# Kernel optimization log

Hardware: AMD Instinct MI355X
Metric: run time of the kernel (lower is better)

The kernel has to match this reference:

```python
import jax, jax.numpy as jnp
import numpy as np

# dims
B, A, CIN, CC = 512, 256, 7, 16          # batch, num_actions, input channels, conv channels
D, H, DH, E = 48, 8, 6, 512              # token_dimension, heads, head_dim, num_embeddings
S, T = 32, 32                            # num_input_tokens, num_output_tokens
AH = H * DH                              # 48
NL = 4                                   # attention layers
CONV_IN = A * CC                         # 4096
ENC = S * D                              # 1536
DEC_OUT = A * CIN                        # 1792
SCALE = float(np.sqrt(D))                # module uses sqrt(input_embedding_dim)
EPS = 1e-5


def _ln(x, g, b):
    m = jnp.mean(x, axis=-1, keepdims=True)
    v = jnp.var(x, axis=-1, keepdims=True)
    return (x - m) * jax.lax.rsqrt(v + EPS) * g + b


def setup_inputs() -> dict:
    key = jax.random.key(0)
    ks = iter(jax.random.split(key, 64))
    def rn(shape, s=0.05):
        return jax.random.normal(next(ks), shape, dtype=jnp.float32) * s
    inp = {}
    inp['x'] = jax.random.normal(next(ks), (B, A, CIN), dtype=jnp.float32)
    inp['u'] = jax.random.uniform(next(ks), (T, B), dtype=jnp.float32)
    inp['bn_g'] = jnp.ones((CIN,), jnp.float32); inp['bn_b'] = jnp.zeros((CIN,), jnp.float32)
    inp['conv_w'] = rn((CC, CIN, 5)); inp['conv_b'] = jnp.zeros((CC,), jnp.float32)
    inp['tk_W1'] = rn((CONV_IN, 2 * CONV_IN)); inp['tk_b1'] = jnp.zeros((2 * CONV_IN,), jnp.float32)
    inp['tk_W2'] = rn((2 * CONV_IN, ENC)); inp['tk_b2'] = jnp.zeros((ENC,), jnp.float32)
    for nm in ('q', 'k', 'v'):
        inp['ln%s_g' % nm] = jnp.ones((NL, D), jnp.float32)
        inp['ln%s_b' % nm] = jnp.zeros((NL, D), jnp.float32)
        inp['W%s' % nm] = rn((NL, D, AH))
        inp['b%s' % nm] = jnp.zeros((NL, AH), jnp.float32)
    inp['Wo'] = rn((NL, AH, D)); inp['bo'] = jnp.zeros((NL, D), jnp.float32)
    inp['mln_g'] = jnp.ones((NL, D), jnp.float32); inp['mln_b'] = jnp.zeros((NL, D), jnp.float32)
    inp['W1'] = rn((NL, D, 2 * D)); inp['b1'] = jnp.zeros((NL, 2 * D), jnp.float32)
    inp['W2'] = rn((NL, 2 * D, D)); inp['b2'] = jnp.zeros((NL, D), jnp.float32)
    inp['emb'] = rn((D, E), 1.0)          # nn.Parameter(torch.randn(D, E))
    inp['pos_enc'] = rn((T, D), 1.0)      # nn.Parameter(torch.randn(T, D))
    inp['dec_W1'] = rn((ENC, 2 * ENC)); inp['dec_b1'] = jnp.zeros((2 * ENC,), jnp.float32)
    inp['dec_W2'] = rn((2 * ENC, DEC_OUT)); inp['dec_b2'] = jnp.zeros((DEC_OUT,), jnp.float32)
    return inp


def _fwd(x, u, bn_g, bn_b, conv_w, conv_b, tk_W1, tk_b1, tk_W2, tk_b2,
         lnq_g, lnq_b, Wq, bq, lnk_g, lnk_b, Wk, bk, lnv_g, lnv_b, Wv, bv, Wo, bo,
         mln_g, mln_b, W1, b1, W2, b2, emb, pos_enc, dec_W1, dec_b1, dec_W2, dec_b2):
    # --- conv stem (BatchNorm1d in training mode: batch statistics) ---
    xt = x.transpose(0, 2, 1)                              # [B, 7, A]
    mu = jnp.mean(xt, axis=(0, 2), keepdims=True)
    var = jnp.var(xt, axis=(0, 2), keepdims=True)
    xn = (xt - mu) * jax.lax.rsqrt(var + EPS) * bn_g[None, :, None] + bn_b[None, :, None]
    xc = jax.lax.conv_general_dilated(xn, conv_w, (1,), ((2, 2),),
                                      dimension_numbers=('NCH', 'OIH', 'NCH')) + conv_b[None, :, None]
    xf = xc.reshape(B, -1)                                 # [B, 16*A]
    h = jax.nn.relu(xf @ tk_W1 + tk_b1)
    toks = (h @ tk_W2 + tk_b2).reshape(B, S, D)            # [B, S, D]

    STOT = S + T
    kc = jnp.zeros((NL, B, H, STOT, DH), jnp.float32)
    vc = jnp.zeros_like(kc)

    # --- prefill pass (output discarded; fills KV caches) ---
    ii = jnp.arange(S)[:, None]; jj = jnp.arange(S)[None, :]
    pre_mask = jnp.where(jj - ii >= S - 1, -999.0, 0.0)    # triu(-999, diagonal=S-1), as in source
    xcur = toks
    for l in range(NL):
        q = (_ln(xcur, lnq_g[l], lnq_b[l]) @ Wq[l] + bq[l]).reshape(B, S, H, DH).transpose(0, 2, 1, 3)
        k = (_ln(xcur, lnk_g[l], lnk_b[l]) @ Wk[l] + bk[l]).reshape(B, S, H, DH).transpose(0, 2, 1, 3)
        v = (_ln(xcur, lnv_g[l], lnv_b[l]) @ Wv[l] + bv[l]).reshape(B, S, H, DH).transpose(0, 2, 1, 3)
        kc = kc.at[l, :, :, :S].set(k)
        vc = vc.at[l, :, :, :S].set(v)
        attn = jax.nn.softmax(jnp.einsum('bhqd,bhkd->bhqk', q, k) / SCALE + pre_mask, axis=-1)
        o = jnp.einsum('bhqk,bhkd->bhqd', attn, v).transpose(0, 2, 1, 3).reshape(B, S, AH)
        xcur = o @ Wo[l] + bo[l] + xcur
        hh = jax.nn.relu(_ln(xcur, mln_g[l], mln_b[l]) @ W1[l] + b1[l])
        xcur = hh @ W2[l] + b2[l]

    jidx = jnp.arange(STOT)

    def step(carry, xs):
        kc, vc = carry
        i, pe, uu = xs
        p = S + i                                          # cache length before this step
        xtk = jnp.broadcast_to(pe, (B, 1, D))
        newk, newv = [], []
        for l in range(NL):
            q = (_ln(xtk, lnq_g[l], lnq_b[l]) @ Wq[l] + bq[l]).reshape(B, 1, H, DH).transpose(0, 2, 1, 3)
            k = (_ln(xtk, lnk_g[l], lnk_b[l]) @ Wk[l] + bk[l]).reshape(B, 1, H, DH).transpose(0, 2, 1, 3)
            v = (_ln(xtk, lnv_g[l], lnv_b[l]) @ Wv[l] + bv[l]).reshape(B, 1, H, DH).transpose(0, 2, 1, 3)
            kcl = jax.lax.dynamic_update_slice(kc[l], k, (0, 0, p, 0))
            vcl = jax.lax.dynamic_update_slice(vc[l], v, (0, 0, p, 0))
            scores = jnp.einsum('bhqd,bhkd->bhqk', q, kcl) / SCALE
            # source mask: -999 added for positions >= mask_offset (includes the new token itself)
            scores = scores + jnp.where(jidx >= p, -999.0, 0.0)
            attn = jax.nn.softmax(scores, axis=-1)
            o = jnp.einsum('bhqk,bhkd->bhqd', attn, vcl).transpose(0, 2, 1, 3).reshape(B, 1, AH)
            xtk = o @ Wo[l] + bo[l] + xtk
            hh = jax.nn.relu(_ln(xtk, mln_g[l], mln_b[l]) @ W1[l] + b1[l])
            xtk = hh @ W2[l] + b2[l]
            newk.append(kcl); newv.append(vcl)
        attended = xtk                                     # [B, 1, D]
        probs = jax.nn.softmax((attended @ emb).reshape(B, E), axis=1)
        cdf = jnp.cumsum(probs, axis=1)
        idx = jnp.clip(jnp.sum((cdf < uu[:, None]).astype(jnp.int32), axis=1), 0, E - 1)
        sel = emb.T[idx].reshape(B, 1, D)
        st = sel + attended - jax.lax.stop_gradient(attended)  # straight-through
        return (jnp.stack(newk), jnp.stack(newv)), st

    (_, _), outs = jax.lax.scan(step, (kc, vc), (jnp.arange(T), pos_enc, u))
    out_tokens = outs.transpose(1, 0, 2, 3).reshape(B, T * D)
    dh_ = jax.nn.relu(out_tokens @ dec_W1 + dec_b1)
    traj = (dh_ @ dec_W2 + dec_b2).reshape(B, A, CIN)
    return traj


def reference(x, u, bn_g, bn_b, conv_w, conv_b, tk_W1, tk_b1, tk_W2, tk_b2,
              lnq_g, lnq_b, Wq, bq, lnk_g, lnk_b, Wk, bk, lnv_g, lnv_b, Wv, bv, Wo, bo,
              mln_g, mln_b, W1, b1, W2, b2, emb, pos_enc, dec_W1, dec_b1, dec_W2, dec_b2):
    return _fwd(x, u, bn_g, bn_b, conv_w, conv_b, tk_W1, tk_b1, tk_W2, tk_b2,
                lnq_g, lnq_b, Wq, bq, lnk_g, lnk_b, Wk, bk, lnv_g, lnv_b, Wv, bv, Wo, bo,
                mln_g, mln_b, W1, b1, W2, b2, emb, pos_enc, dec_W1, dec_b1, dec_W2, dec_b2)
```

## Files before the change

kernel.cpp:

```cpp
#include <hip/hip_runtime.h>

static const double SCALE_ = 6.928203230275509;

__device__ inline float  fma_t(float a, float b, float c)  { return fmaf(a, b, c); }
__device__ inline double fma_t(double a, double b, double c){ return fma(a, b, c); }

__device__ __attribute__((noinline)) double dotW(const double* a,
                                                 const float* W, int n, int ldw,
                                                 double init) {
  double a0 = init, a1 = 0.0;
#pragma unroll 2
  for (int i = 0; i < n; i += 2) {
    a0 = fma(a[i],     (double)W[i * ldw],       a0);
    a1 = fma(a[i + 1], (double)W[(i + 1) * ldw], a1);
  }
  return a0 + a1;
}

template <int N, typename WP>
__device__ __forceinline__ double dotN(const double* a, WP W, int ldw, double init) {
  double c0 = init, c1 = 0.0, c2 = 0.0, c3 = 0.0;
#pragma unroll
  for (int i = 0; i < N; i += 4) {
    c0 = fma(a[i],     (double)W[i * ldw],       c0);
    c1 = fma(a[i + 1], (double)W[(i + 1) * ldw], c1);
    c2 = fma(a[i + 2], (double)W[(i + 2) * ldw], c2);
    c3 = fma(a[i + 3], (double)W[(i + 3) * ldw], c3);
  }
  return (c0 + c1) + (c2 + c3);
}

__device__ __attribute__((noinline)) double2 ln_stats48(const double* x) {
  double s0 = 0, s1 = 0, q0 = 0, q1 = 0;
#pragma unroll 2
  for (int i = 0; i < 48; i += 2) {
    const double va = x[i], vb = x[i + 1];
    s0 += va; q0 = fma(va, va, q0);
    s1 += vb; q1 = fma(vb, vb, q1);
  }
  const double m = (s0 + s1) / 48.0;
  const double rs = 1.0 / sqrt((q0 + q1) / 48.0 - m * m + 1e-5);
  return make_double2(m, rs);
}

__device__ __attribute__((noinline)) double exp_ni(double x) { return exp(x); }

__global__ __launch_bounds__(256) void bn_partial_kernel(const float* __restrict__ x,
                                                         double* __restrict__ part) {
  __shared__ double sh[256 * 14];
  const int tid = threadIdx.x;
  const int idx = blockIdx.x * 256 + tid;
  const float* p = x + (size_t)idx * 7;
  for (int c = 0; c < 7; ++c) {
    double v = (double)p[c];
    sh[tid * 14 + c] = v;
    sh[tid * 14 + 7 + c] = v * v;
  }
  __syncthreads();
  if (tid < 14) {
    double acc = 0.0;
    for (int t = 0; t < 256; ++t) acc += sh[t * 14 + tid];
    part[blockIdx.x * 14 + tid] = acc;
  }
}

__global__ void bn_final_kernel(const double* __restrict__ part,
                                const float* __restrict__ g, const float* __restrict__ bb,
                                double* __restrict__ stat) {
  const int c = threadIdx.x;
  if (c < 7) {
    double s = 0.0, s2 = 0.0;
    for (int i = 0; i < 512; ++i) { s += part[i * 14 + c]; s2 += part[i * 14 + 7 + c]; }
    const double mean = s / 131072.0;
    const double var = s2 / 131072.0 - mean * mean;
    const double rstd = 1.0 / sqrt(var + 1e-5);
    const double scale = rstd * (double)g[c];
    stat[c] = scale;
    stat[7 + c] = (double)bb[c] - mean * scale;
  }
}

__global__ __launch_bounds__(256) void conv_kernel(const float* __restrict__ x,
                                                   const float* __restrict__ wconv,
                                                   const float* __restrict__ cb,
                                                   const double* __restrict__ stat,
                                                   double* __restrict__ xf) {
  __shared__ double wsh[560 + 14];
  const int tid = threadIdx.x;
  for (int i = tid; i < 560; i += 256) wsh[i] = (double)wconv[i];
  for (int i = tid; i < 14; i += 256) wsh[560 + i] = stat[i];
  __syncthreads();
  const int idx = blockIdx.x * 256 + tid;
  const int a = idx & 255;
  const int o = (idx >> 8) & 15;
  const int b = idx >> 12;
  double acc = (double)cb[o];
  const float* xb = x + (size_t)b * (256 * 7);
  for (int k = 0; k < 5; ++k) {
    const int pos = a + k - 2;
    if (pos < 0 || pos >= 256) continue;
    const float* xp = xb + pos * 7;
    for (int ci = 0; ci < 7; ++ci) {
      const double xn = (double)xp[ci] * wsh[560 + ci] + wsh[567 + ci];
      acc = fma(xn, wsh[(o * 7 + ci) * 5 + k], acc);
    }
  }
  xf[idx] = acc;
}

template <typename T, bool BIAS, bool RELU>
__global__ __launch_bounds__(256) void gemm128_kernel(const T* __restrict__ A,
                                                      const float* __restrict__ Bm,
                                                      const float* __restrict__ bias,
                                                      T* __restrict__ C,
                                                      const int M, const int N, const int K,
                                                      const int kc) {
  __shared__ T As[16][130];
  __shared__ T Bs[16][66];
  const int tid = threadIdx.x;
  const int tx = tid & 15, ty = tid >> 4;
  const int n0 = blockIdx.x * 64, m0 = blockIdx.y * 128;
  const int k0 = blockIdx.z * kc, kend = k0 + kc;
  const int ar = tid >> 1, ac = (tid & 1) * 8;
  const int br = tid >> 4, bc = (tid & 15) * 4;
  const T* Ap = A + (size_t)(m0 + ar) * K;
  const float* Bp = Bm + (size_t)br * N + n0 + bc;
  T acc[8][4] = {};
  for (int k = k0; k < kend; k += 16) {
    T av8[8];
#pragma unroll
    for (int i = 0; i < 8; ++i) av8[i] = Ap[k + ac + i];
    const float4 bw = *(const float4*)(Bp + (size_t)k * N);
#pragma unroll
    for (int i = 0; i < 8; ++i) As[ac + i][ar] = av8[i];
    Bs[br][bc] = (T)bw.x; Bs[br][bc + 1] = (T)bw.y;
    Bs[br][bc + 2] = (T)bw.z; Bs[br][bc + 3] = (T)bw.w;
    __syncthreads();
#pragma unroll
    for (int kk = 0; kk < 16; ++kk) {
      T a[8], b[4];
#pragma unroll
      for (int i = 0; i < 8; ++i) a[i] = As[kk][ty * 8 + i];
#pragma unroll
      for (int j = 0; j < 4; ++j) b[j] = Bs[kk][tx * 4 + j];
#pragma unroll
      for (int i = 0; i < 8; ++i)
#pragma unroll
        for (int j = 0; j < 4; ++j) acc[i][j] = fma_t(a[i], b[j], acc[i][j]);
    }
    __syncthreads();
  }
  T* Cp = C + (size_t)blockIdx.z * M * N;
#pragma unroll
  for (int i = 0; i < 8; ++i) {
    const int row = m0 + ty * 8 + i;
#pragma unroll
    for (int j = 0; j < 4; ++j) {
      const int col = n0 + tx * 4 + j;
      T v = acc[i][j];
      if (BIAS) v += (T)bias[col];
      if (RELU) v = v > (T)0 ? v : (T)0;
      Cp[(size_t)row * N + col] = v;
    }
  }
}

template <typename T, bool BIAS, bool RELU>
__global__ __launch_bounds__(256) void gemm_kernel(const T* __restrict__ A,
                                                   const float* __restrict__ Bm,
                                                   const float* __restrict__ bias,
                                                   T* __restrict__ C,
                                                   const int M, const int N, const int K,
                                                   const int kc) {
  __shared__ T As[16][65];
  __shared__ T Bs[16][65];
  const int tid = threadIdx.x;
  const int tx = tid & 15, ty = tid >> 4;
  const int n0 = blockIdx.x * 64, m0 = blockIdx.y * 64;
  const int k0 = blockIdx.z * kc, kend = k0 + kc;
  const int ar = tid >> 2, ac = (tid & 3) * 4;
  const int br = tid >> 4, bc = (tid & 15) * 4;
  const T* Ap = A + (size_t)(m0 + ar) * K;
  const float* Bp = Bm + (size_t)br * N + n0 + bc;
  T acc[4][4] = {};
  for (int k = k0; k < kend; k += 16) {
    const T a0 = Ap[k + ac], a1 = Ap[k + ac + 1], a2 = Ap[k + ac + 2], a3 = Ap[k + ac + 3];
    const float4 bw = *(const float4*)(Bp + (size_t)k * N);
    As[ac][ar] = a0; As[ac + 1][ar] = a1; As[ac + 2][ar] = a2; As[ac + 3][ar] = a3;
    Bs[br][bc] = (T)bw.x; Bs[br][bc + 1] = (T)bw.y; Bs[br][bc + 2] = (T)bw.z; Bs[br][bc + 3] = (T)bw.w;
    __syncthreads();
#pragma unroll
    for (int kk = 0; kk < 16; ++kk) {
      T av[4], bv2[4];
#pragma unroll
      for (int i = 0; i < 4; ++i) av[i] = As[kk][ty * 4 + i];
#pragma unroll
      for (int j = 0; j < 4; ++j) bv2[j] = Bs[kk][tx * 4 + j];
#pragma unroll
      for (int i = 0; i < 4; ++i)
#pragma unroll
        for (int j = 0; j < 4; ++j) acc[i][j] = fma_t(av[i], bv2[j], acc[i][j]);
    }
    __syncthreads();
  }
  T* Cp = C + (size_t)blockIdx.z * M * N;
#pragma unroll
  for (int i = 0; i < 4; ++i) {
    const int row = m0 + ty * 4 + i;
#pragma unroll
    for (int j = 0; j < 4; ++j) {
      const int col = n0 + tx * 4 + j;
      T v = acc[i][j];
      if (BIAS) v += (T)bias[col];
      if (RELU) v = v > (T)0 ? v : (T)0;
      Cp[(size_t)row * N + col] = v;
    }
  }
}

__global__ __launch_bounds__(256) void reduce2_bias_kernel(const double* __restrict__ part,
                                                           const float* __restrict__ bias,
                                                           double* __restrict__ out,
                                                           const int MN, const int N) {
  const int i = blockIdx.x * 256 + threadIdx.x;
  if (i < MN) out[i] = part[i] + part[MN + i] + (double)bias[i % N];
}

__global__ __launch_bounds__(256) void prefill_kernel(
    const double* __restrict__ toks,
    const float* __restrict__ lnq_g, const float* __restrict__ lnq_b,
    const float* __restrict__ Wq, const float* __restrict__ bq,
    const float* __restrict__ lnk_g, const float* __restrict__ lnk_b,
    const float* __restrict__ Wk, const float* __restrict__ bk,
    const float* __restrict__ lnv_g, const float* __restrict__ lnv_b,
    const float* __restrict__ Wv, const float* __restrict__ bvv,
    const float* __restrict__ Wo, const float* __restrict__ bo,
    const float* __restrict__ mln_g, const float* __restrict__ mln_b,
    const float* __restrict__ W1, const float* __restrict__ b1,
    const float* __restrict__ W2, const float* __restrict__ b2,
    double* __restrict__ kcache, double* __restrict__ vcache) {
  const int b = blockIdx.x, tid = threadIdx.x;
  __shared__ double xcur[1536], abuf[1536], qbuf[1536], kvbuf[3072];
  __shared__ double mean[32], rstd[32];
  double* kb = kvbuf;
  double* vb = kvbuf + 1536;

#pragma unroll 1
  for (int i = tid; i < 1536; i += 256) xcur[i] = toks[(size_t)b * 1536 + i];
  __syncthreads();

#pragma unroll 1
  for (int l = 0; l < 4; ++l) {
    if (tid < 32) {
      double s = 0.0, s2 = 0.0;
#pragma unroll 4
      for (int i = 0; i < 48; ++i) { const double v = xcur[tid * 48 + i]; s += v; s2 += v * v; }
      const double m = s / 48.0;
      mean[tid] = m;
      rstd[tid] = 1.0 / sqrt(s2 / 48.0 - m * m + 1e-5);
    }
    __syncthreads();
    const bool last = (l == 3);

    if (!last) {
#pragma unroll 1
      for (int i = tid; i < 1536; i += 256) {
        const int t = i / 48, d = i % 48;
        abuf[i] = (xcur[i] - mean[t]) * rstd[t] * (double)lnq_g[l * 48 + d] + (double)lnq_b[l * 48 + d];
      }
      __syncthreads();
#pragma unroll 1
      for (int i = tid; i < 1536; i += 256) {
        const int t = i / 48, j = i % 48;
        qbuf[i] = dotW(abuf + t * 48, Wq + l * 2304 + j, 48, 48, (double)bq[l * 48 + j]);
      }
      __syncthreads();
    }
#pragma unroll 1
    for (int i = tid; i < 1536; i += 256) {
      const int t = i / 48, d = i % 48;
      abuf[i] = (xcur[i] - mean[t]) * rstd[t] * (double)lnk_g[l * 48 + d] + (double)lnk_b[l * 48 + d];
    }
    __syncthreads();
#pragma unroll 1
    for (int i = tid; i < 1536; i += 256) {
      const int t = i / 48, j = i % 48;
      kb[i] = dotW(abuf + t * 48, Wk + l * 2304 + j, 48, 48, (double)bk[l * 48 + j]);
    }
    __syncthreads();
#pragma unroll 1
    for (int i = tid; i < 1536; i += 256) {
      const int t = i / 48, d = i % 48;
      abuf[i] = (xcur[i] - mean[t]) * rstd[t] * (double)lnv_g[l * 48 + d] + (double)lnv_b[l * 48 + d];
    }
    __syncthreads();
#pragma unroll 1
    for (int i = tid; i < 1536; i += 256) {
      const int t = i / 48, j = i % 48;
      vb[i] = dotW(abuf + t * 48, Wv + l * 2304 + j, 48, 48, (double)bvv[l * 48 + j]);
    }
    __syncthreads();
#pragma unroll 1
    for (int i = tid; i < 1536; i += 256) {
      const int t = i / 48, j = i % 48;
      const int h = j / 6, d = j % 6;
      const size_t ci = ((((size_t)b * 4 + l) * 8 + h) * 64 + t) * 6 + d;
      kcache[ci] = kb[i];
      vcache[ci] = vb[i];
    }

    if (!last) {
      const int t = tid >> 3, h = tid & 7;
      const double* qp = qbuf + t * 48 + h * 6;
      const double q0 = qp[0], q1 = qp[1], q2 = qp[2], q3 = qp[3], q4 = qp[4], q5 = qp[5];
      double mx = -1e300;
#pragma unroll 4
      for (int j = 0; j < 32; ++j) {
        const double* kp = kb + j * 48 + h * 6;
        double sv = q0 * kp[0];
        sv = fma(q1, kp[1], sv); sv = fma(q2, kp[2], sv); sv = fma(q3, kp[3], sv);
        sv = fma(q4, kp[4], sv); sv = fma(q5, kp[5], sv);
        sv /= SCALE_;
        if (t == 0 && j == 31) sv -= 999.0;
        mx = sv > mx ? sv : mx;
      }
      double den = 0, o0 = 0, o1 = 0, o2 = 0, o3 = 0, o4 = 0, o5 = 0;
#pragma unroll 4
      for (int j = 0; j < 32; ++j) {
        const double* kp = kb + j * 48 + h * 6;
        double sv = q0 * kp[0];
        sv = fma(q1, kp[1], sv); sv = fma(q2, kp[2], sv); sv = fma(q3, kp[3], sv);
        sv = fma(q4, kp[4], sv); sv = fma(q5, kp[5], sv);
        sv /= SCALE_;
        if (t == 0 && j == 31) sv -= 999.0;
        const double e = exp_ni(sv - mx);
        den += e;
        const double* vp = vb + j * 48 + h * 6;
        o0 = fma(e, vp[0], o0); o1 = fma(e, vp[1], o1); o2 = fma(e, vp[2], o2);
        o3 = fma(e, vp[3], o3); o4 = fma(e, vp[4], o4); o5 = fma(e, vp[5], o5);
      }
      abuf[t * 48 + h * 6 + 0] = o0 / den;
      abuf[t * 48 + h * 6 + 1] = o1 / den;
      abuf[t * 48 + h * 6 + 2] = o2 / den;
      abuf[t * 48 + h * 6 + 3] = o3 / den;
      abuf[t * 48 + h * 6 + 4] = o4 / den;
      abuf[t * 48 + h * 6 + 5] = o5 / den;
      __syncthreads();
#pragma unroll 1
      for (int i = tid; i < 1536; i += 256) {
        const int t2 = i / 48, j = i % 48;
        xcur[i] += dotW(abuf + t2 * 48, Wo + l * 2304 + j, 48, 48, (double)bo[l * 48 + j]);
      }
      __syncthreads();
      if (tid < 32) {
        double s = 0.0, s2 = 0.0;
#pragma unroll 4
        for (int i = 0; i < 48; ++i) { const double v = xcur[tid * 48 + i]; s += v; s2 += v * v; }
        const double m = s / 48.0;
        mean[tid] = m;
        rstd[tid] = 1.0 / sqrt(s2 / 48.0 - m * m + 1e-5);
      }
      __syncthreads();
#pragma unroll 1
      for (int i = tid; i < 1536; i += 256) {
        const int t2 = i / 48, d = i % 48;
        qbuf[i] = (xcur[i] - mean[t2]) * rstd[t2] * (double)mln_g[l * 48 + d] + (double)mln_b[l * 48 + d];
      }
      __syncthreads();
#pragma unroll 1
      for (int i = tid; i < 3072; i += 256) {
        const int t2 = i / 96, jj = i % 96;
        const double acc = dotW(qbuf + t2 * 48, W1 + l * 4608 + jj, 48, 96, (double)b1[l * 96 + jj]);
        kvbuf[i] = acc > 0 ? acc : 0;
      }
      __syncthreads();
#pragma unroll 1
      for (int i = tid; i < 1536; i += 256) {
        const int t2 = i / 48, j = i % 48;
        abuf[i] = dotW(kvbuf + t2 * 96, W2 + l * 4608 + j, 96, 48, (double)b2[l * 48 + j]);
      }
      __syncthreads();
#pragma unroll 1
      for (int i = tid; i < 1536; i += 256) xcur[i] = abuf[i];
      __syncthreads();
    }
  }
}

__device__ __attribute__((noinline)) void sample_step(
    double* xtk, double* probs, double* red,
    const float* __restrict__ emb, const float* __restrict__ u,
    float* __restrict__ out_tok, int b, int step, int tid) {
  const double lg1 = dotN<48>(xtk, emb + tid, 512, 0.0);
  const double lg2 = dotN<48>(xtk, emb + 256 + tid, 512, 0.0);
  double mx = lg1 > lg2 ? lg1 : lg2;
#pragma unroll
  for (int off = 1; off < 64; off <<= 1) { const double o2 = __shfl_xor(mx, off); mx = o2 > mx ? o2 : mx; }
  if ((tid & 63) == 0) red[tid >> 6] = mx;
  __syncthreads();
  {
    const double m0 = red[0] > red[1] ? red[0] : red[1];
    const double m1 = red[2] > red[3] ? red[2] : red[3];
    mx = m0 > m1 ? m0 : m1;
  }
  probs[tid] = exp(lg1 - mx);
  probs[tid + 256] = exp(lg2 - mx);
  __syncthreads();
  if (tid < 64) {
    const int lane = tid;
    double loc[8], run = 0;
#pragma unroll
    for (int n2 = 0; n2 < 8; ++n2) { run += probs[lane * 8 + n2]; loc[n2] = run; }
    double incl = run;
#pragma unroll
    for (int off = 1; off < 64; off <<= 1) {
      const double t2 = __shfl_up(incl, off);
      if (lane >= off) incl += t2;
    }
    const double excl = incl - run;
    const double Ssum = __shfl(incl, 63);
    const double uu = (double)u[step * 512 + b];
    int cnt = 0;
#pragma unroll
    for (int n2 = 0; n2 < 8; ++n2) cnt += ((excl + loc[n2]) / Ssum < uu) ? 1 : 0;
#pragma unroll
    for (int off = 1; off < 64; off <<= 1) cnt += __shfl_xor(cnt, off);
    const int idx = cnt > 511 ? 511 : cnt;
    if (lane < 48) {
      const double sel = (double)emb[lane * 512 + idx];
      const double att = xtk[lane];
      out_tok[(size_t)b * 1536 + step * 48 + lane] = (float)((sel + att) - att);
    }
  }
  __syncthreads();
}

__global__ __launch_bounds__(256) void ar_kernel(
    const float* __restrict__ pos_enc, const float* __restrict__ u,
    const float* __restrict__ lnq_g, const float* __restrict__ lnq_b,
    const float* __restrict__ Wq, const float* __restrict__ bq,
    const float* __restrict__ lnk_g, const float* __restrict__ lnk_b,
    const float* __restrict__ Wk, const float* __restrict__ bk,
    const float* __restrict__ lnv_g, const float* __restrict__ lnv_b,
    const float* __restrict__ Wv, const float* __restrict__ bvv,
    const float* __restrict__ Wo, const float* __restrict__ bo,
    const float* __restrict__ mln_g, const float* __restrict__ mln_b,
    const float* __restrict__ W1, const float* __restrict__ b1,
    const float* __restrict__ W2, const float* __restrict__ b2,
    const float* __restrict__ emb,
    double* __restrict__ kcache, double* __restrict__ vcache,
    float* __restrict__ out_tok) {
  const int b = blockIdx.x, tid = threadIdx.x;
  __shared__ double xtk[48], anorm[144], qs[48], os[48], hh[96], probs[512], red[4];
  __shared__ float wsh[9216];

#pragma unroll 1
  for (int step = 0; step < 32; ++step) {
    const int p = 32 + step;
    if (tid < 48) xtk[tid] = (double)pos_enc[step * 48 + tid];
    __syncthreads();

#pragma unroll 1
    for (int l = 0; l < 4; ++l) {
      {
        float4* wsh4 = (float4*)wsh;
#pragma unroll 1
        for (int i = tid; i < 2304; i += 256) {
          const int a = i / 576, off4 = i - a * 576;
          const float* src = a == 0 ? Wq : a == 1 ? Wk : a == 2 ? Wv : Wo;
          wsh4[i] = ((const float4*)(src + l * 2304))[off4];
        }
      }
      {
        const double2 st = ln_stats48(xtk);
        if (tid < 144) {
          const int which = tid / 48, d = tid - which * 48;
          const float* gp = which == 0 ? lnq_g : which == 1 ? lnk_g : lnv_g;
          const float* bp = which == 0 ? lnq_b : which == 1 ? lnk_b : lnv_b;
          anorm[tid] = (xtk[d] - st.x) * st.y * (double)gp[l * 48 + d] + (double)bp[l * 48 + d];
        }
      }
      __syncthreads();
      if (tid < 144) {
        const int which = tid / 48, j = tid - which * 48;
        const float* bbp = which == 0 ? bq : which == 1 ? bk : bvv;
        const double acc = dotN<48>(anorm + which * 48, wsh + which * 2304 + j, 48,
                                    (double)bbp[l * 48 + j]);
        if (which == 0) {
          qs[j] = acc;
        } else {
          const int h = j / 6, d = j - h * 6;
          const size_t ci = ((((size_t)b * 4 + l) * 8 + h) * 64 + p) * 6 + d;
          if (which == 1) kcache[ci] = acc; else vcache[ci] = acc;
        }
      }
      __syncthreads();
      {
        const int h = tid >> 5, r = tid & 31;
        const double* kcb = kcache + ((((size_t)b * 4 + l) * 8 + h) * 64) * 6;
        const double* vcb = vcache + ((((size_t)b * 4 + l) * 8 + h) * 64) * 6;
        const double qv0 = qs[h * 6 + 0], qv1 = qs[h * 6 + 1], qv2 = qs[h * 6 + 2],
                     qv3 = qs[h * 6 + 3], qv4 = qs[h * 6 + 4], qv5 = qs[h * 6 + 5];
        const bool has2 = (r + 32) < p;
        const double* kp1 = kcb + r * 6;
        double sv1 = qv0 * kp1[0];
        sv1 = fma(qv1, kp1[1], sv1); sv1 = fma(qv2, kp1[2], sv1); sv1 = fma(qv3, kp1[3], sv1);
        sv1 = fma(qv4, kp1[4], sv1); sv1 = fma(qv5, kp1[5], sv1);
        sv1 /= SCALE_;
        double sv2 = -1e300;
        if (has2) {
          const double* kp2 = kcb + (r + 32) * 6;
          double t2 = qv0 * kp2[0];
          t2 = fma(qv1, kp2[1], t2); t2 = fma(qv2, kp2[2], t2); t2 = fma(qv3, kp2[3], t2);
          t2 = fma(qv4, kp2[4], t2); t2 = fma(qv5, kp2[5], t2);
          sv2 = t2 / SCALE_;
        }
        double mx = sv1 > sv2 ? sv1 : sv2;
#pragma unroll
        for (int off = 1; off < 32; off <<= 1) { const double o2 = __shfl_xor(mx, off); mx = o2 > mx ? o2 : mx; }
        const double e1 = exp(sv1 - mx);
        const double e2 = has2 ? exp(sv2 - mx) : 0.0;
        double den = e1 + e2;
        const double* vp1 = vcb + r * 6;
        double o[6];
#pragma unroll
        for (int d = 0; d < 6; ++d) o[d] = e1 * vp1[d];
        if (has2) {
          const double* vp2 = vcb + (r + 32) * 6;
#pragma unroll
          for (int d = 0; d < 6; ++d) o[d] = fma(e2, vp2[d], o[d]);
        }
#pragma unroll
        for (int off = 1; off < 32; off <<= 1) {
          den += __shfl_xor(den, off);
#pragma unroll
          for (int d = 0; d < 6; ++d) o[d] += __shfl_xor(o[d], off);
        }
        if (r == 0) {
#pragma unroll
          for (int d = 0; d < 6; ++d) os[h * 6 + d] = o[d] / den;
        }
      }
      __syncthreads();
      if (tid < 48)
        xtk[tid] += dotN<48>(os, wsh + 3 * 2304 + tid, 48, (double)bo[l * 48 + tid]);
      __syncthreads();
      {
        float4* wsh4 = (float4*)wsh;
#pragma unroll 1
        for (int i = tid; i < 2304; i += 256) {
          const int a = i / 1152, off4 = i - a * 1152;
          const float* src = a == 0 ? W1 : W2;
          wsh4[i] = ((const float4*)(src + l * 4608))[off4];
        }
      }
      {
        const double2 st = ln_stats48(xtk);
        if (tid < 48)
          anorm[tid] = (xtk[tid] - st.x) * st.y * (double)mln_g[l * 48 + tid] + (double)mln_b[l * 48 + tid];
      }
      __syncthreads();
      if (tid < 96) {
        const double v = dotN<48>(anorm, wsh + tid, 96, (double)b1[l * 96 + tid]);
        hh[tid] = v > 0 ? v : 0;
      }
      __syncthreads();
      if (tid < 48)
        xtk[tid] = dotN<96>(hh, wsh + 4608 + tid, 48, (double)b2[l * 48 + tid]);
      __syncthreads();
    }

    sample_step(xtk, probs, red, emb, u, out_tok, b, step, tid);
  }
}

extern "C" void kernel_launch(void* const* d_in, const int* in_sizes, int n_in,
                              void* d_out, int out_size, void* d_ws, size_t ws_size,
                              hipStream_t stream) {
  const float* x      = (const float*)d_in[0];
  const float* u      = (const float*)d_in[1];
  const float* bn_g   = (const float*)d_in[2];
  const float* bn_b   = (const float*)d_in[3];
  const float* conv_w = (const float*)d_in[4];
  const float* conv_b = (const float*)d_in[5];
  const float* tk_W1  = (const float*)d_in[6];
  const float* tk_b1  = (const float*)d_in[7];
  const float* tk_W2  = (const float*)d_in[8];
  const float* tk_b2  = (const float*)d_in[9];
  const float* lnq_g  = (const float*)d_in[10];
  const float* lnq_b  = (const float*)d_in[11];
  const float* Wq     = (const float*)d_in[12];
  const float* bq     = (const float*)d_in[13];
  const float* lnk_g  = (const float*)d_in[14];
  const float* lnk_b  = (const float*)d_in[15];
  const float* Wk     = (const float*)d_in[16];
  const float* bk     = (const float*)d_in[17];
  const float* lnv_g  = (const float*)d_in[18];
  const float* lnv_b  = (const float*)d_in[19];
  const float* Wv     = (const float*)d_in[20];
  const float* bvv    = (const float*)d_in[21];
  const float* Wo     = (const float*)d_in[22];
  const float* bo     = (const float*)d_in[23];
  const float* mln_g  = (const float*)d_in[24];
  const float* mln_b  = (const float*)d_in[25];
  const float* W1     = (const float*)d_in[26];
  const float* b1     = (const float*)d_in[27];
  const float* W2     = (const float*)d_in[28];
  const float* b2     = (const float*)d_in[29];
  const float* emb    = (const float*)d_in[30];
  const float* pos    = (const float*)d_in[31];
  const float* dW1    = (const float*)d_in[32];
  const float* db1    = (const float*)d_in[33];
  const float* dW2    = (const float*)d_in[34];
  const float* db2    = (const float*)d_in[35];
  float* out = (float*)d_out;

  char* w = (char*)d_ws;
  size_t off = 0;
  auto alloc = [&](size_t bytes) {
    size_t o = off;
    off = (off + bytes + 255) & ~(size_t)255;
    return o;
  };
  const size_t o_bnp  = alloc(512 * 14 * 8);
  const size_t o_bns  = alloc(14 * 8);
  const size_t o_xf   = alloc(16777216);
  const size_t o_h    = alloc(33554432);
  const size_t o_toks = alloc(6291456);
  const size_t o_kc   = alloc(50331648);
  const size_t o_vc   = alloc(50331648);

  double* bnp  = (double*)(w + o_bnp);
  double* bns  = (double*)(w + o_bns);
  double* xf   = (double*)(w + o_xf);
  double* hbuf = (double*)(w + o_h);
  double* toks = (double*)(w + o_toks);
  double* kc   = (double*)(w + o_kc);
  double* vc   = (double*)(w + o_vc);
  double* part = (double*)(w + o_xf);
  float*  otok = (float*)(w + o_h);
  float*  dh   = (float*)(w + o_h + 4194304);

  bn_partial_kernel<<<512, 256, 0, stream>>>(x, bnp);
  bn_final_kernel<<<1, 64, 0, stream>>>(bnp, bn_g, bn_b, bns);
  conv_kernel<<<8192, 256, 0, stream>>>(x, conv_w, conv_b, bns, xf);
  gemm128_kernel<double, true, true><<<dim3(128, 4, 1), 256, 0, stream>>>(
      xf, tk_W1, tk_b1, hbuf, 512, 8192, 4096, 4096);
  gemm128_kernel<double, false, false><<<dim3(24, 4, 2), 256, 0, stream>>>(
      hbuf, tk_W2, nullptr, part, 512, 1536, 8192, 4096);
  reduce2_bias_kernel<<<3072, 256, 0, stream>>>(part, tk_b2, toks, 512 * 1536, 1536);
  prefill_kernel<<<512, 256, 0, stream>>>(toks,
      lnq_g, lnq_b, Wq, bq, lnk_g, lnk_b, Wk, bk, lnv_g, lnv_b, Wv, bvv,
      Wo, bo, mln_g, mln_b, W1, b1, W2, b2, kc, vc);
  ar_kernel<<<512, 256, 0, stream>>>(pos, u,
      lnq_g, lnq_b, Wq, bq, lnk_g, lnk_b, Wk, bk, lnv_g, lnv_b, Wv, bvv,
      Wo, bo, mln_g, mln_b, W1, b1, W2, b2, emb, kc, vc, otok);
  gemm_kernel<float, true, true><<<dim3(48, 8, 1), 256, 0, stream>>>(
      otok, dW1, db1, dh, 512, 3072, 1536, 1536);
  gemm_kernel<float, true, false><<<dim3(28, 8, 1), 256, 0, stream>>>(
      dh, dW2, db2, out, 512, 1792, 3072, 3072);
}
```

Before: 5.000 ms.

## Shrink autoregressive kernel to one wavefront with pre-transposed global weights

Adds a kernel that transposes the attention, MLP and embedding weights so each output's row is contiguous and can be read with float4 loads. The autoregressive kernel now runs with 64 threads per block instead of 256. It drops the per-layer staging of weights into shared memory, keeps only the small LayerNorm and bias parameters in LDS, and reads weights straight from global memory or cache. Attention and sampling are reorganised so one wavefront does them with fewer block-wide barriers. The cost is less parallelism per block, more work per thread, and an extra transpose launch.

Result: slower. 5.288 ms (+5.8%).

```diff
diff --git a/kernel.cpp b/kernel.cpp
--- a/kernel.cpp
+++ b/kernel.cpp
@@ -17,15 +17,28 @@
   return a0 + a1;
 }
 
-template <int N, typename WP>
-__device__ __forceinline__ double dotN(const double* a, WP W, int ldw, double init) {
+__device__ __forceinline__ double dot48_row(const double* a, const float* Wrow, double init) {
   double c0 = init, c1 = 0.0, c2 = 0.0, c3 = 0.0;
 #pragma unroll
-  for (int i = 0; i < N; i += 4) {
-    c0 = fma(a[i],     (double)W[i * ldw],       c0);
-    c1 = fma(a[i + 1], (double)W[(i + 1) * ldw], c1);
-    c2 = fma(a[i + 2], (double)W[(i + 2) * ldw], c2);
-    c3 = fma(a[i + 3], (double)W[(i + 3) * ldw], c3);
+  for (int i = 0; i < 48; i += 4) {
+    const float4 wv = *(const float4*)(Wrow + i);
+    c0 = fma(a[i],     (double)wv.x, c0);
+    c1 = fma(a[i + 1], (double)wv.y, c1);
+    c2 = fma(a[i + 2], (double)wv.z, c2);
+    c3 = fma(a[i + 3], (double)wv.w, c3);
+  }
+  return (c0 + c1) + (c2 + c3);
+}
+
+__device__ __forceinline__ double dot96_row(const double* a, const float* Wrow, double init) {
+  double c0 = init, c1 = 0.0, c2 = 0.0, c3 = 0.0;
+#pragma unroll
+  for (int i = 0; i < 96; i += 4) {
+    const float4 wv = *(const float4*)(Wrow + i);
+    c0 = fma(a[i],     (double)wv.x, c0);
+    c1 = fma(a[i + 1], (double)wv.y, c1);
+    c2 = fma(a[i + 2], (double)wv.z, c2);
+    c3 = fma(a[i + 3], (double)wv.w, c3);
   }
   return (c0 + c1) + (c2 + c3);
 }
@@ -226,6 +239,40 @@
   if (i < MN) out[i] = part[i] + part[MN + i] + (double)bias[i % N];
 }
 
+__global__ __launch_bounds__(256) void transpose_weights_kernel(
+    const float* __restrict__ Wq, const float* __restrict__ Wk,
+    const float* __restrict__ Wv, const float* __restrict__ Wo,
+    const float* __restrict__ W1, const float* __restrict__ W2,
+    const float* __restrict__ emb,
+    float* __restrict__ WqT, float* __restrict__ WkT,
+    float* __restrict__ WvT, float* __restrict__ WoT,
+    float* __restrict__ W1T, float* __restrict__ W2T,
+    float* __restrict__ embT) {
+  const int t = blockIdx.x * 256 + threadIdx.x;
+  if (t < 36864) {
+    const int a = t / 9216, r = t - a * 9216;
+    const int l = r / 2304, e = r - l * 2304;
+    const int i = e / 48, j = e - i * 48;
+    const float* src = a == 0 ? Wq : a == 1 ? Wk : a == 2 ? Wv : Wo;
+    float* dst = a == 0 ? WqT : a == 1 ? WkT : a == 2 ? WvT : WoT;
+    dst[l * 2304 + j * 48 + i] = src[l * 2304 + i * 48 + j];
+  } else if (t < 55296) {
+    const int t1 = t - 36864;
+    const int l = t1 / 4608, e = t1 - l * 4608;
+    const int i = e / 96, j = e - i * 96;
+    W1T[l * 4608 + j * 48 + i] = W1[l * 4608 + i * 96 + j];
+  } else if (t < 73728) {
+    const int t2 = t - 55296;
+    const int l = t2 / 4608, e = t2 - l * 4608;
+    const int i = e / 48, j = e - i * 48;
+    W2T[l * 4608 + j * 96 + i] = W2[l * 4608 + i * 48 + j];
+  } else {
+    const int t3 = t - 73728;
+    const int d = t3 / 512, e = t3 - d * 512;
+    embT[e * 48 + d] = emb[d * 512 + e];
+  }
+}
+
 __global__ __launch_bounds__(256) void prefill_kernel(
     const double* __restrict__ toks,
     const float* __restrict__ lnq_g, const float* __restrict__ lnq_b,
@@ -387,72 +434,36 @@
   }
 }
 
-__device__ __attribute__((noinline)) void sample_step(
-    double* xtk, double* probs, double* red,
-    const float* __restrict__ emb, const float* __restrict__ u,
-    float* __restrict__ out_tok, int b, int step, int tid) {
-  const double lg1 = dotN<48>(xtk, emb + tid, 512, 0.0);
-  const double lg2 = dotN<48>(xtk, emb + 256 + tid, 512, 0.0);
-  double mx = lg1 > lg2 ? lg1 : lg2;
-#pragma unroll
-  for (int off = 1; off < 64; off <<= 1) { const double o2 = __shfl_xor(mx, off); mx = o2 > mx ? o2 : mx; }
-  if ((tid & 63) == 0) red[tid >> 6] = mx;
-  __syncthreads();
-  {
-    const double m0 = red[0] > red[1] ? red[0] : red[1];
-    const double m1 = red[2] > red[3] ? red[2] : red[3];
-    mx = m0 > m1 ? m0 : m1;
-  }
-  probs[tid] = exp(lg1 - mx);
-  probs[tid + 256] = exp(lg2 - mx);
-  __syncthreads();
-  if (tid < 64) {
-    const int lane = tid;
-    double loc[8], run = 0;
-#pragma unroll
-    for (int n2 = 0; n2 < 8; ++n2) { run += probs[lane * 8 + n2]; loc[n2] = run; }
-    double incl = run;
-#pragma unroll
-    for (int off = 1; off < 64; off <<= 1) {
-      const double t2 = __shfl_up(incl, off);
-      if (lane >= off) incl += t2;
-    }
-    const double excl = incl - run;
-    const double Ssum = __shfl(incl, 63);
-    const double uu = (double)u[step * 512 + b];
-    int cnt = 0;
-#pragma unroll
-    for (int n2 = 0; n2 < 8; ++n2) cnt += ((excl + loc[n2]) / Ssum < uu) ? 1 : 0;
-#pragma unroll
-    for (int off = 1; off < 64; off <<= 1) cnt += __shfl_xor(cnt, off);
-    const int idx = cnt > 511 ? 511 : cnt;
-    if (lane < 48) {
-      const double sel = (double)emb[lane * 512 + idx];
-      const double att = xtk[lane];
-      out_tok[(size_t)b * 1536 + step * 48 + lane] = (float)((sel + att) - att);
-    }
-  }
-  __syncthreads();
-}
-
-__global__ __launch_bounds__(256) void ar_kernel(
+__global__ __launch_bounds__(64, 1) void ar_kernel(
     const float* __restrict__ pos_enc, const float* __restrict__ u,
     const float* __restrict__ lnq_g, const float* __restrict__ lnq_b,
-    const float* __restrict__ Wq, const float* __restrict__ bq,
+    const float* __restrict__ WqT, const float* __restrict__ bq,
     const float* __restrict__ lnk_g, const float* __restrict__ lnk_b,
-    const float* __restrict__ Wk, const float* __restrict__ bk,
+    const float* __restrict__ WkT, const float* __restrict__ bk,
     const float* __restrict__ lnv_g, const float* __restrict__ lnv_b,
-    const float* __restrict__ Wv, const float* __restrict__ bvv,
-    const float* __restrict__ Wo, const float* __restrict__ bo,
+    const float* __restrict__ WvT, const float* __restrict__ bvv,
+    const float* __restrict__ WoT, const float* __restrict__ bo,
     const float* __restrict__ mln_g, const float* __restrict__ mln_b,
-    const float* __restrict__ W1, const float* __restrict__ b1,
-    const float* __restrict__ W2, const float* __restrict__ b2,
-    const float* __restrict__ emb,
+    const float* __restrict__ W1T, const float* __restrict__ b1,
+    const float* __restrict__ W2T, const float* __restrict__ b2,
+    const float* __restrict__ embT,
     double* __restrict__ kcache, double* __restrict__ vcache,
     float* __restrict__ out_tok) {
   const int b = blockIdx.x, tid = threadIdx.x;
-  __shared__ double xtk[48], anorm[144], qs[48], os[48], hh[96], probs[512], red[4];
-  __shared__ float wsh[9216];
+  __shared__ double xtk[48], anorm[144], qs[48], os[48], hh[96];
+  __shared__ float par[2880];
+  {
+    const float* srcs[14] = {lnq_g, lnq_b, lnk_g, lnk_b, lnv_g, lnv_b, mln_g, mln_b,
+                             bq, bk, bvv, bo, b1, b2};
+    const int sz[14] = {192, 192, 192, 192, 192, 192, 192, 192, 192, 192, 192, 192, 384, 192};
+    int base = 0;
+#pragma unroll 1
+    for (int a2 = 0; a2 < 14; ++a2) {
+      for (int i = tid; i < sz[a2]; i += 64) par[base + i] = srcs[a2][i];
+      base += sz[a2];
+    }
+  }
+  __syncthreads();
 
 #pragma unroll 1
   for (int step = 0; step < 32; ++step) {
@@ -463,29 +474,23 @@
 #pragma unroll 1
     for (int l = 0; l < 4; ++l) {
       {
-        float4* wsh4 = (float4*)wsh;
-#pragma unroll 1
-        for (int i = tid; i < 2304; i += 256) {
-          const int a = i / 576, off4 = i - a * 576;
-          const float* src = a == 0 ? Wq : a == 1 ? Wk : a == 2 ? Wv : Wo;
-          wsh4[i] = ((const float4*)(src + l * 2304))[off4];
+        const double2 st = ln_stats48(xtk);
+#pragma unroll
+        for (int i = tid; i < 144; i += 64) {
+          const int which = i / 48, d = i - which * 48;
+          const float* gp = par + 384 * which;
+          const float* bp = gp + 192;
+          anorm[i] = (xtk[d] - st.x) * st.y * (double)gp[l * 48 + d] + (double)bp[l * 48 + d];
         }
       }
-      {
-        const double2 st = ln_stats48(xtk);
-        if (tid < 144) {
-          const int which = tid / 48, d = tid - which * 48;
-          const float* gp = which == 0 ? lnq_g : which == 1 ? lnk_g : lnv_g;
-          const float* bp = which == 0 ? lnq_b : which == 1 ? lnk_b : lnv_b;
-          anorm[tid] = (xtk[d] - st.x) * st.y * (double)gp[l * 48 + d] + (double)bp[l * 48 + d];
-        }
-      }
-      __syncthreads();
-      if (tid < 144) {
-        const int which = tid / 48, j = tid - which * 48;
-        const float* bbp = which == 0 ? bq : which == 1 ? bk : bvv;
-        const double acc = dotN<48>(anorm + which * 48, wsh + which * 2304 + j, 48,
-                                    (double)bbp[l * 48 + j]);
+      __syncthreads();
+#pragma unroll
+      for (int i = tid; i < 144; i += 64) {
+        const int which = i / 48, j = i - which * 48;
+        const float* WT = which == 0 ? WqT : which == 1 ? WkT : WvT;
+        const float* bbp = par + 1536 + 192 * which;
+        const double acc = dot48_row(anorm + which * 48, WT + l * 2304 + j * 48,
+                                     (double)bbp[l * 48 + j]);
         if (which == 0) {
           qs[j] = acc;
         } else {
@@ -496,81 +501,110 @@
       }
       __syncthreads();
       {
-        const int h = tid >> 5, r = tid & 31;
+        const int h = tid >> 3, rl = tid & 7;
         const double* kcb = kcache + ((((size_t)b * 4 + l) * 8 + h) * 64) * 6;
         const double* vcb = vcache + ((((size_t)b * 4 + l) * 8 + h) * 64) * 6;
-        const double qv0 = qs[h * 6 + 0], qv1 = qs[h * 6 + 1], qv2 = qs[h * 6 + 2],
-                     qv3 = qs[h * 6 + 3], qv4 = qs[h * 6 + 4], qv5 = qs[h * 6 + 5];
-        const bool has2 = (r + 32) < p;
-        const double* kp1 = kcb + r * 6;
-        double sv1 = qv0 * kp1[0];
-        sv1 = fma(qv1, kp1[1], sv1); sv1 = fma(qv2, kp1[2], sv1); sv1 = fma(qv3, kp1[3], sv1);
-        sv1 = fma(qv4, kp1[4], sv1); sv1 = fma(qv5, kp1[5], sv1);
-        sv1 /= SCALE_;
-        double sv2 = -1e300;
-        if (has2) {
-          const double* kp2 = kcb + (r + 32) * 6;
-          double t2 = qv0 * kp2[0];
-          t2 = fma(qv1, kp2[1], t2); t2 = fma(qv2, kp2[2], t2); t2 = fma(qv3, kp2[3], t2);
-          t2 = fma(qv4, kp2[4], t2); t2 = fma(qv5, kp2[5], t2);
-          sv2 = t2 / SCALE_;
+        double qv[6];
+#pragma unroll
+        for (int d = 0; d < 6; ++d) qv[d] = qs[h * 6 + d];
+        double sv[8];
+        double mx = -1e300;
+        int nk = 0;
+#pragma unroll 2
+        for (int r = rl; r < p; r += 8) {
+          const double* kp = kcb + r * 6;
+          double s = qv[0] * kp[0];
+          s = fma(qv[1], kp[1], s); s = fma(qv[2], kp[2], s); s = fma(qv[3], kp[3], s);
+          s = fma(qv[4], kp[4], s); s = fma(qv[5], kp[5], s);
+          s /= SCALE_;
+          sv[nk++] = s;
+          mx = s > mx ? s : mx;
         }
-        double mx = sv1 > sv2 ? sv1 : sv2;
-#pragma unroll
-        for (int off = 1; off < 32; off <<= 1) { const double o2 = __shfl_xor(mx, off); mx = o2 > mx ? o2 : mx; }
-        const double e1 = exp(sv1 - mx);
-        const double e2 = has2 ? exp(sv2 - mx) : 0.0;
-        double den = e1 + e2;
-        const double* vp1 = vcb + r * 6;
-        double o[6];
-#pragma unroll
-        for (int d = 0; d < 6; ++d) o[d] = e1 * vp1[d];
-        if (has2) {
-          const double* vp2 = vcb + (r + 32) * 6;
-#pragma unroll
-          for (int d = 0; d < 6; ++d) o[d] = fma(e2, vp2[d], o[d]);
+#pragma unroll
+        for (int off = 1; off < 8; off <<= 1) {
+          const double o2 = __shfl_xor(mx, off); mx = o2 > mx ? o2 : mx;
         }
-#pragma unroll
-        for (int off = 1; off < 32; off <<= 1) {
+        double den = 0.0, o[6] = {0, 0, 0, 0, 0, 0};
+        int kk = 0;
+#pragma unroll 2
+        for (int r = rl; r < p; r += 8) {
+          const double e = exp(sv[kk++] - mx);
+          den += e;
+          const double* vp = vcb + r * 6;
+#pragma unroll
+          for (int d = 0; d < 6; ++d) o[d] = fma(e, vp[d], o[d]);
+        }
+#pragma unroll
+        for (int off = 1; off < 8; off <<= 1) {
           den += __shfl_xor(den, off);
 #pragma unroll
           for (int d = 0; d < 6; ++d) o[d] += __shfl_xor(o[d], off);
         }
-        if (r == 0) {
+        if (rl == 0) {
 #pragma unroll
           for (int d = 0; d < 6; ++d) os[h * 6 + d] = o[d] / den;
         }
       }
       __syncthreads();
       if (tid < 48)
-        xtk[tid] += dotN<48>(os, wsh + 3 * 2304 + tid, 48, (double)bo[l * 48 + tid]);
-      __syncthreads();
-      {
-        float4* wsh4 = (float4*)wsh;
-#pragma unroll 1
-        for (int i = tid; i < 2304; i += 256) {
-          const int a = i / 1152, off4 = i - a * 1152;
-          const float* src = a == 0 ? W1 : W2;
-          wsh4[i] = ((const float4*)(src + l * 4608))[off4];
-        }
-      }
+        xtk[tid] += dot48_row(os, WoT + l * 2304 + tid * 48, (double)par[2112 + l * 48 + tid]);
+      __syncthreads();
       {
         const double2 st = ln_stats48(xtk);
         if (tid < 48)
-          anorm[tid] = (xtk[tid] - st.x) * st.y * (double)mln_g[l * 48 + tid] + (double)mln_b[l * 48 + tid];
-      }
-      __syncthreads();
-      if (tid < 96) {
-        const double v = dotN<48>(anorm, wsh + tid, 96, (double)b1[l * 96 + tid]);
-        hh[tid] = v > 0 ? v : 0;
+          anorm[tid] = (xtk[tid] - st.x) * st.y * (double)par[1152 + l * 48 + tid]
+                       + (double)par[1344 + l * 48 + tid];
+      }
+      __syncthreads();
+#pragma unroll
+      for (int j = tid; j < 96; j += 64) {
+        const double v2 = dot48_row(anorm, W1T + l * 4608 + j * 48, (double)par[2304 + l * 96 + j]);
+        hh[j] = v2 > 0 ? v2 : 0;
       }
       __syncthreads();
       if (tid < 48)
-        xtk[tid] = dotN<96>(hh, wsh + 4608 + tid, 48, (double)b2[l * 48 + tid]);
-      __syncthreads();
-    }
-
-    sample_step(xtk, probs, red, emb, u, out_tok, b, step, tid);
+        xtk[tid] = dot96_row(hh, W2T + l * 4608 + tid * 96, (double)par[2688 + l * 48 + tid]);
+      __syncthreads();
+    }
+
+    {
+      double lg[8];
+      const float* er = embT + (size_t)tid * 384;
+      double mx = -1e300;
+#pragma unroll 2
+      for (int n = 0; n < 8; ++n) {
+        lg[n] = dot48_row(xtk, er + n * 48, 0.0);
+        mx = lg[n] > mx ? lg[n] : mx;
+      }
+#pragma unroll
+      for (int off = 1; off < 64; off <<= 1) {
+        const double o2 = __shfl_xor(mx, off); mx = o2 > mx ? o2 : mx;
+      }
+      double loc[8], run = 0.0;
+#pragma unroll
+      for (int n = 0; n < 8; ++n) { run += exp(lg[n] - mx); loc[n] = run; }
+      double incl = run;
+#pragma unroll
+      for (int off = 1; off < 64; off <<= 1) {
+        const double t2 = __shfl_up(incl, off);
+        if (tid >= off) incl += t2;
+      }
+      const double excl = incl - run;
+      const double Ssum = __shfl(incl, 63);
+      const double uu = (double)u[step * 512 + b];
+      int cnt = 0;
+#pragma unroll
+      for (int n = 0; n < 8; ++n) cnt += ((excl + loc[n]) / Ssum < uu) ? 1 : 0;
+#pragma unroll
+      for (int off = 1; off < 64; off <<= 1) cnt += __shfl_xor(cnt, off);
+      const int idx = cnt > 511 ? 511 : cnt;
+      if (tid < 48) {
+        const double sel = (double)embT[(size_t)idx * 48 + tid];
+        const double att = xtk[tid];
+        out_tok[(size_t)b * 1536 + step * 48 + tid] = (float)((sel + att) - att);
+      }
+    }
+    __syncthreads();
   }
 }
 
@@ -640,6 +674,13 @@
   double* part = (double*)(w + o_xf);
   float*  otok = (float*)(w + o_h);
   float*  dh   = (float*)(w + o_h + 4194304);
+  float* WqT  = (float*)(w + o_h + 16777216);
+  float* WkT  = WqT + 9216;
+  float* WvT  = WkT + 9216;
+  float* WoT  = WvT + 9216;
+  float* W1T  = WoT + 9216;
+  float* W2T  = W1T + 18432;
+  float* embT = W2T + 18432;
 
   bn_partial_kernel<<<512, 256, 0, stream>>>(x, bnp);
   bn_final_kernel<<<1, 64, 0, stream>>>(bnp, bn_g, bn_b, bns);
@@ -649,12 +690,14 @@
   gemm128_kernel<double, false, false><<<dim3(24, 4, 2), 256, 0, stream>>>(
       hbuf, tk_W2, nullptr, part, 512, 1536, 8192, 4096);
   reduce2_bias_kernel<<<3072, 256, 0, stream>>>(part, tk_b2, toks, 512 * 1536, 1536);
+  transpose_weights_kernel<<<384, 256, 0, stream>>>(Wq, Wk, Wv, Wo, W1, W2, emb,
+      WqT, WkT, WvT, WoT, W1T, W2T, embT);
   prefill_kernel<<<512, 256, 0, stream>>>(toks,
       lnq_g, lnq_b, Wq, bq, lnk_g, lnk_b, Wk, bk, lnv_g, lnv_b, Wv, bvv,
       Wo, bo, mln_g, mln_b, W1, b1, W2, b2, kc, vc);
-  ar_kernel<<<512, 256, 0, stream>>>(pos, u,
-      lnq_g, lnq_b, Wq, bq, lnk_g, lnk_b, Wk, bk, lnv_g, lnv_b, Wv, bvv,
-      Wo, bo, mln_g, mln_b, W1, b1, W2, b2, emb, kc, vc, otok);
+  ar_kernel<<<512, 64, 0, stream>>>(pos, u,
+      lnq_g, lnq_b, WqT, bq, lnk_g, lnk_b, WkT, bk, lnv_g, lnv_b, WvT, bvv,
+      WoT, bo, mln_g, mln_b, W1T, b1, W2T, b2, embT, kc, vc, otok);
   gemm_kernel<float, true, true><<<dim3(48, 8, 1), 256, 0, stream>>>(
       otok, dW1, db1, dh, 512, 3072, 1536, 1536);
   gemm_kernel<float, true, false><<<dim3(28, 8, 1), 256, 0, stream>>>(
```
